# Performance work log

Hardware: AMD Instinct MI355X
Metric: run time of the kernel (lower is better)

Reference implementation:

```python
import jax, jax.numpy as jnp
import numpy as np

L = 2        # n_layers
IN = 172     # in_channels
HID = 128    # hidden_channels
NH = 4       # heads
HD = HID // NH  # per-head dim = 32
TD = 100     # time_dim
V = 400000   # global node table size
N = 150000   # sampled subgraph nodes
E = 500000   # edges per layer
B = 15000    # seed batch size


def setup_inputs() -> dict:
    key = jax.random.key(0)
    ks = jax.random.split(key, 24)
    p = lambda k, shp, s=0.05: jax.random.normal(k, shp, jnp.float32) * s
    inp = {
        "x_all": jax.random.normal(ks[0], (V, IN), jnp.float32),
        "all_node_ids": jax.random.randint(ks[1], (N,), 0, V),
        "edge_src": jax.random.randint(ks[2], (L, E), 0, N),
        "edge_dst": jax.random.randint(ks[3], (L, E), 0, N),
        "dts": jax.random.uniform(ks[4], (L, E), jnp.float32, 0.0, 1e4),
        "batch_size": B,
        # TimeEncode params
        "basis_freq": jnp.asarray(1.0 / 10 ** np.linspace(0, 9, TD), jnp.float32),
        "phase": jnp.zeros((TD,), jnp.float32),
        # input projection
        "Wp": p(ks[5], (IN, HID)), "bp": jnp.zeros((HID,), jnp.float32),
        # per-layer TransformerConv params (stacked over L)
        "Wq": p(ks[6], (L, HID, HID)), "bq": jnp.zeros((L, HID), jnp.float32),
        "Wk": p(ks[7], (L, HID, HID)), "bk": jnp.zeros((L, HID), jnp.float32),
        "Wv": p(ks[8], (L, HID, HID)), "bv": jnp.zeros((L, HID), jnp.float32),
        "We": p(ks[9], (L, TD, HID)),  # lin_edge, bias=False in PyG
        "Wskip": p(ks[10], (L, HID, HID)), "bskip": jnp.zeros((L, HID), jnp.float32),
        "bn_g": jnp.ones((L, HID), jnp.float32), "bn_b": jnp.zeros((L, HID), jnp.float32),
        # classifier head
        "W1": p(ks[11], (HID, HID)), "b1": jnp.zeros((HID,), jnp.float32),
        "g1": jnp.ones((HID,), jnp.float32), "be1": jnp.zeros((HID,), jnp.float32),
        "W2": p(ks[12], (HID, HID // 2)), "b2": jnp.zeros((HID // 2,), jnp.float32),
        "g2": jnp.ones((HID // 2,), jnp.float32), "be2": jnp.zeros((HID // 2,), jnp.float32),
        "W3": p(ks[13], (HID // 2, 1)), "b3": jnp.zeros((1,), jnp.float32),
    }
    return inp


def _bn(x, g, b):
    # BatchNorm1d, training-mode batch statistics (biased variance), eps=1e-5
    m = x.mean(0)
    v = x.var(0)
    return g * (x - m) * jax.lax.rsqrt(v + 1e-5) + b


def reference(x_all, all_node_ids, edge_src, edge_dst, dts, batch_size,
              basis_freq, phase, Wp, bp, Wq, bq, Wk, bk, Wv, bv, We,
              Wskip, bskip, bn_g, bn_b, W1, b1, g1, be1, W2, b2, g2, be2, W3, b3):
    n = all_node_ids.shape[0]
    x = x_all[all_node_ids]                      # [N, IN] gather from global table
    h = jax.nn.relu(x @ Wp + bp)                 # [N, HID]
    inv_sqrt_d = 1.0 / np.sqrt(HD)
    for i in range(L):
        src, dst, dt = edge_src[i], edge_dst[i], dts[i]
        # learnable sinusoidal time encoding of edge delta-t  [E, TD]
        te = jnp.cos(dt[:, None] * basis_freq[None, :] + phase[None, :])
        q = (h @ Wq[i] + bq[i]).reshape(n, NH, HD)
        k = (h @ Wk[i] + bk[i]).reshape(n, NH, HD)
        v = (h @ Wv[i] + bv[i]).reshape(n, NH, HD)
        e = (te @ We[i]).reshape(-1, NH, HD)     # [E, NH, HD]
        kj = k[src] + e                          # key + edge proj (PyG TransformerConv)
        vj = v[src] + e                          # value + edge proj
        alpha = jnp.einsum('ehd,ehd->eh', q[dst], kj) * inv_sqrt_d  # [E, NH]
        # scatter-softmax over edges grouped by destination node
        m = jax.ops.segment_max(alpha, dst, num_segments=n)
        a = jnp.exp(alpha - m[dst])
        s = jax.ops.segment_sum(a, dst, num_segments=n) + 1e-16
        w = a / s[dst]                           # [E, NH]
        agg = jax.ops.segment_sum(w[:, :, None] * vj, dst, num_segments=n)
        out = agg.reshape(n, HID) + h @ Wskip[i] + bskip[i]  # concat heads + root skip
        h = _bn(jax.nn.relu(out), bn_g[i], bn_b[i])          # dropout = identity (eval)
    hb = h[:batch_size]
    z = jax.nn.relu(_bn(hb @ W1 + b1, g1, be1))
    z = jax.nn.relu(_bn(z @ W2 + b2, g2, be2))
    return (z @ W3 + b3)[:, 0]                   # [batch_size]
```

## Files before the change

kernel.cpp:

```cpp
#include <hip/hip_runtime.h>
#include <hip/hip_bf16.h>
#include <math.h>

#define IN_DIM 172
#define HID 128
#define TDIM 100
#define KPAD 192

typedef __attribute__((ext_vector_type(8))) short bf16x8;
typedef __attribute__((ext_vector_type(4))) float f32x4;

static __device__ __forceinline__ ushort f2b(float x) {
  unsigned u = __float_as_uint(x);
  u += 0x7FFFu + ((u >> 16) & 1u);
  return (ushort)(u >> 16);
}
static __device__ __forceinline__ float blo(unsigned w) { return __uint_as_float(w << 16); }
static __device__ __forceinline__ float bhi(unsigned w) { return __uint_as_float(w & 0xffff0000u); }

__global__ void k_wpt(const float* __restrict__ Wp, ushort* __restrict__ wpt) {
  int i = blockIdx.x * 256 + threadIdx.x;
  if (i >= 128 * KPAD) return;
  int c = i / KPAD, k = i - c * KPAD;
  wpt[i] = (k < IN_DIM) ? f2b(Wp[k * HID + c]) : (ushort)0;
}

__global__ __launch_bounds__(256) void k_in_mfma(
    const float* __restrict__ x_all, const int* __restrict__ ids,
    const ushort* __restrict__ wpt, const float* __restrict__ bp,
    ushort* __restrict__ h, int n) {
  __shared__ __align__(16) ushort xs[64][200];
  int tid = threadIdx.x;
  long r0 = (long)blockIdx.x * 64;
  for (int i = tid; i < 64 * 28; i += 256) {
    int r = i / 28, c = IN_DIM + (i - r * 28);
    xs[r][c] = 0;
  }
  for (int i = tid; i < 64 * 43; i += 256) {
    int r = i / 43, seg = i - r * 43;
    long row = r0 + r;
    float4 v = make_float4(0.f, 0.f, 0.f, 0.f);
    if (row < n) v = *(const float4*)(x_all + (size_t)ids[row] * IN_DIM + seg * 4);
    ushort4 u;
    u.x = f2b(v.x); u.y = f2b(v.y); u.z = f2b(v.z); u.w = f2b(v.w);
    *(ushort4*)&xs[r][seg * 4] = u;
  }
  __syncthreads();
  int wv = tid >> 6, l = tid & 63;
  int arow = wv * 16 + (l & 15);
  int kb0 = (l >> 4) * 8;
  bf16x8 a[6];
  #pragma unroll
  for (int kk = 0; kk < 6; ++kk) a[kk] = *(const bf16x8*)&xs[arow][kk * 32 + kb0];
  #pragma unroll
  for (int nt = 0; nt < 8; ++nt) {
    int col = nt * 16 + (l & 15);
    const ushort* wcol = wpt + (size_t)col * KPAD + kb0;
    f32x4 acc = {0.f, 0.f, 0.f, 0.f};
    #pragma unroll
    for (int kk = 0; kk < 6; ++kk) {
      bf16x8 bfr = *(const bf16x8*)(wcol + kk * 32);
      acc = __builtin_amdgcn_mfma_f32_16x16x32_bf16(a[kk], bfr, acc, 0, 0, 0);
    }
    float bias = bp[col];
    #pragma unroll
    for (int j = 0; j < 4; ++j) {
      long row = r0 + wv * 16 + (l >> 4) * 4 + j;
      if (row < n) {
        float y = acc[j] + bias;
        h[row * HID + col] = f2b(y > 0.f ? y : 0.f);
      }
    }
  }
}

__global__ void k_wprep(const float* __restrict__ Wq, const float* __restrict__ Wk,
                        const float* __restrict__ Wv, const float* __restrict__ Ws,
                        const float* __restrict__ bq, const float* __restrict__ bk,
                        const float* __restrict__ bv, const float* __restrict__ bs,
                        ushort* __restrict__ wallT, float* __restrict__ ball) {
  int i = blockIdx.x * 256 + threadIdx.x;
  if (i >= 512 * 128) return;
  int col = i >> 7, k = i & 127;
  int m = col >> 7, c = col & 127;
  const float* W = (m == 0) ? Wq : (m == 1) ? Wk : (m == 2) ? Wv : Ws;
  wallT[i] = f2b(W[k * HID + c]);
  if (k == 0) {
    const float* bb = (m == 0) ? bq : (m == 1) ? bk : (m == 2) ? bv : bs;
    ball[col] = bb[c];
  }
}

__global__ void k_wt128(const float* __restrict__ W, ushort* __restrict__ wt) {
  int i = blockIdx.x * 256 + threadIdx.x;
  if (i >= 128 * 128) return;
  int c = i >> 7, k = i & 127;
  wt[i] = f2b(W[k * HID + c]);
}

__global__ __launch_bounds__(512) void k_qkvs(
    const ushort* __restrict__ h, const ushort* __restrict__ wallT,
    const float* __restrict__ ball,
    ushort* __restrict__ qb, ushort* __restrict__ kbuf, ushort* __restrict__ vb,
    float* __restrict__ ob, int n) {
  __shared__ __align__(16) ushort hs[128][136];
  __shared__ __align__(16) ushort ws[64][136];
  int tid = threadIdx.x;
  long r0 = (long)blockIdx.x * 128;
  bf16x8 zv = {0, 0, 0, 0, 0, 0, 0, 0};
  for (int i = tid; i < 128 * 16; i += 512) {
    int r = i >> 4, cseg = i & 15;
    long row = r0 + r;
    bf16x8 v = (row < n) ? *(const bf16x8*)&h[row * HID + cseg * 8] : zv;
    *(bf16x8*)&hs[r][cseg * 8] = v;
  }
  __syncthreads();
  int wv = tid >> 6, l = tid & 63;
  int arow = wv * 16 + (l & 15);
  int kb0 = (l >> 4) * 8;
  bf16x8 a[4];
  #pragma unroll
  for (int kk = 0; kk < 4; ++kk) a[kk] = *(const bf16x8*)&hs[arow][kk * 32 + kb0];

  for (int g = 0; g < 8; ++g) {
    __syncthreads();
    for (int i = tid; i < 64 * 16; i += 512) {
      int c = i >> 4, cseg = i & 15;
      *(bf16x8*)&ws[c][cseg * 8] =
          *(const bf16x8*)&wallT[(size_t)(g * 64 + c) * 128 + cseg * 8];
    }
    __syncthreads();
    #pragma unroll
    for (int nt = 0; nt < 4; ++nt) {
      int colc = nt * 16 + (l & 15);
      int gcol = g * 64 + colc;
      f32x4 acc = {0.f, 0.f, 0.f, 0.f};
      #pragma unroll
      for (int kk = 0; kk < 4; ++kk) {
        bf16x8 bfr = *(const bf16x8*)&ws[colc][kk * 32 + kb0];
        acc = __builtin_amdgcn_mfma_f32_16x16x32_bf16(a[kk], bfr, acc, 0, 0, 0);
      }
      float bias = ball[gcol];
      int m = gcol >> 7, c = gcol & 127;
      #pragma unroll
      for (int j = 0; j < 4; ++j) {
        long row = r0 + wv * 16 + (l >> 4) * 4 + j;
        if (row < n) {
          float y = acc[j] + bias;
          if (m == 3) ob[row * HID + c] = y;
          else {
            ushort* db = (m == 0) ? qb : (m == 1) ? kbuf : vb;
            db[row * HID + c] = f2b(y);
          }
        }
      }
    }
  }
}

__global__ __launch_bounds__(256) void k_mfma128(
    const ushort* __restrict__ X, const ushort* __restrict__ WT,
    const float* __restrict__ bias, float* __restrict__ Y, int n) {
  __shared__ __align__(16) ushort hs[64][136];
  int tid = threadIdx.x;
  long r0 = (long)blockIdx.x * 64;
  bf16x8 zv = {0, 0, 0, 0, 0, 0, 0, 0};
  for (int i = tid; i < 64 * 16; i += 256) {
    int r = i >> 4, cseg = i & 15;
    long row = r0 + r;
    bf16x8 v = (row < n) ? *(const bf16x8*)&X[row * HID + cseg * 8] : zv;
    *(bf16x8*)&hs[r][cseg * 8] = v;
  }
  __syncthreads();
  int wv = tid >> 6, l = tid & 63;
  int arow = wv * 16 + (l & 15);
  int kb0 = (l >> 4) * 8;
  bf16x8 a[4];
  #pragma unroll
  for (int kk = 0; kk < 4; ++kk) a[kk] = *(const bf16x8*)&hs[arow][kk * 32 + kb0];
  #pragma unroll
  for (int nt = 0; nt < 8; ++nt) {
    int col = nt * 16 + (l & 15);
    const ushort* wcol = WT + (size_t)col * 128 + kb0;
    f32x4 acc = {0.f, 0.f, 0.f, 0.f};
    #pragma unroll
    for (int kk = 0; kk < 4; ++kk) {
      bf16x8 bfr = *(const bf16x8*)(wcol + kk * 32);
      acc = __builtin_amdgcn_mfma_f32_16x16x32_bf16(a[kk], bfr, acc, 0, 0, 0);
    }
    float bs = bias[col];
    #pragma unroll
    for (int j = 0; j < 4; ++j) {
      long row = r0 + wv * 16 + (l >> 4) * 4 + j;
      if (row < n) Y[row * HID + col] = acc[j] + bs;
    }
  }
}

__global__ void k_hist(const int* __restrict__ dst, int* __restrict__ counts, int nE) {
  int e = blockIdx.x * 256 + threadIdx.x;
  if (e < nE) atomicAdd(&counts[dst[e]], 1);
}

__global__ void k_scan_chunk(const int* __restrict__ counts, int* __restrict__ offs,
                             int* __restrict__ chunkSums, int n) {
  __shared__ int ls[256];
  int t = threadIdx.x;
  int base = blockIdx.x * 1024 + t * 4;
  int v[4];
  #pragma unroll
  for (int j = 0; j < 4; ++j) v[j] = (base + j < n) ? counts[base + j] : 0;
  ls[t] = v[0] + v[1] + v[2] + v[3];
  __syncthreads();
  for (int off = 1; off < 256; off <<= 1) {
    int x = (t >= off) ? ls[t - off] : 0;
    __syncthreads();
    ls[t] += x;
    __syncthreads();
  }
  int run = (t == 0) ? 0 : ls[t - 1];
  if (t == 255) chunkSums[blockIdx.x] = ls[255];
  #pragma unroll
  for (int j = 0; j < 4; ++j) {
    if (base + j < n) offs[base + j] = run;
    run += v[j];
  }
}

__global__ void k_scan_tops(int* __restrict__ chunkSums, int nchunks) {
  __shared__ int ls[256];
  int t = threadIdx.x;
  ls[t] = (t < nchunks) ? chunkSums[t] : 0;
  __syncthreads();
  for (int off = 1; off < 256; off <<= 1) {
    int x = (t >= off) ? ls[t - off] : 0;
    __syncthreads();
    ls[t] += x;
    __syncthreads();
  }
  int excl = (t == 0) ? 0 : ls[t - 1];
  if (t < nchunks) chunkSums[t] = excl;
}

__global__ void k_scan_add(int* __restrict__ offs, const int* __restrict__ chunkSums,
                           int n, int nE) {
  int i = blockIdx.x * 256 + threadIdx.x;
  if (i < n) offs[i] += chunkSums[i >> 10];
  if (i == 0) offs[n] = nE;
}

__global__ void k_scatter(const int* __restrict__ src, const int* __restrict__ dst,
                          const float* __restrict__ dts, const int* __restrict__ offs,
                          int* __restrict__ cursor, int* __restrict__ src_s,
                          float* __restrict__ dts_s, int nE) {
  int e = blockIdx.x * 256 + threadIdx.x;
  if (e >= nE) return;
  int d = dst[e];
  int pos = offs[d] + atomicAdd(&cursor[d], 1);
  src_s[pos] = src[e];
  dts_s[pos] = dts[e];
}

__global__ void k_wet(const float* __restrict__ We, ushort* __restrict__ wet) {
  int i = blockIdx.x * 256 + threadIdx.x;
  if (i >= 128 * 128) return;
  int c = i >> 7, t = i & 127;
  wet[i] = (t < TDIM) ? f2b(We[t * HID + c]) : (ushort)0;
}

__global__ __launch_bounds__(256) void k_te_mfma(
    const float* __restrict__ dts, const float* __restrict__ freq,
    const float* __restrict__ phase, const ushort* __restrict__ wet,
    ushort* __restrict__ eb, int nE) {
  __shared__ __align__(16) ushort te[64][136];
  __shared__ float dt_s[64];
  __shared__ float fr_s[128], ph_s[128];
  int tid = threadIdx.x;
  if (tid < 128) {
    fr_s[tid] = (tid < TDIM) ? freq[tid] : 0.f;
    ph_s[tid] = (tid < TDIM) ? phase[tid] : 0.f;
  }
  long e0 = (long)blockIdx.x << 6;
  if (tid < 64) dt_s[tid] = (e0 + tid < nE) ? dts[e0 + tid] : 0.f;
  __syncthreads();
  for (int i = tid; i < 64 * 128; i += 256) {
    int el = i >> 7, t = i & 127;
    float val = (t < TDIM) ? __cosf(dt_s[el] * fr_s[t] + ph_s[t]) : 0.f;
    te[el][t] = f2b(val);
  }
  __syncthreads();
  int wv = tid >> 6, l = tid & 63;
  int arow = wv * 16 + (l & 15);
  int kb0 = (l >> 4) * 8;
  bf16x8 a[4];
  #pragma unroll
  for (int kk = 0; kk < 4; ++kk) a[kk] = *(const bf16x8*)&te[arow][kk * 32 + kb0];
  #pragma unroll
  for (int nt = 0; nt < 8; ++nt) {
    int col = nt * 16 + (l & 15);
    const ushort* wcol = wet + (size_t)col * 128 + kb0;
    f32x4 acc = {0.f, 0.f, 0.f, 0.f};
    #pragma unroll
    for (int kk = 0; kk < 4; ++kk) {
      bf16x8 bfr = *(const bf16x8*)(wcol + kk * 32);
      acc = __builtin_amdgcn_mfma_f32_16x16x32_bf16(a[kk], bfr, acc, 0, 0, 0);
    }
    #pragma unroll
    for (int j = 0; j < 4; ++j) {
      long row = e0 + wv * 16 + (l >> 4) * 4 + j;
      if (row < nE) eb[row * 128 + col] = f2b(acc[j]);
    }
  }
}

__global__ void k_attn(const int* __restrict__ offs, const int* __restrict__ src_s,
                       const ushort* __restrict__ eb, const ushort* __restrict__ qb,
                       const ushort* __restrict__ kb, const ushort* __restrict__ vb,
                       float* __restrict__ ob, int n) {
  int d = (blockIdx.x * 256 + threadIdx.x) >> 6;
  if (d >= n) return;
  int lane = threadIdx.x & 63;
  int half = lane >> 5;
  int cl = lane & 31;
  int c0 = cl * 4;
  int beg = offs[d], end = offs[d + 1];
  if (beg == end) return;
  uint2 qw = *(const uint2*)(qb + (size_t)d * HID + c0);
  float q0 = blo(qw.x), q1 = bhi(qw.x), q2 = blo(qw.y), q3 = bhi(qw.y);
  float m = -INFINITY, s = 0.f;
  float a0 = 0.f, a1 = 0.f, a2 = 0.f, a3 = 0.f;
  for (int base = beg; base < end; base += 2) {
    int pos = base + half;
    bool valid = pos < end;
    int pp = valid ? pos : end - 1;
    int sv = src_s[pp];
    uint2 kw = *(const uint2*)(kb + (size_t)sv * HID + c0);
    uint2 vw = *(const uint2*)(vb + (size_t)sv * HID + c0);
    uint2 ew = *(const uint2*)(eb + (size_t)pp * HID + c0);
    float e0v = blo(ew.x), e1v = bhi(ew.x), e2v = blo(ew.y), e3v = bhi(ew.y);
    float p = q0 * (blo(kw.x) + e0v) + q1 * (bhi(kw.x) + e1v) +
              q2 * (blo(kw.y) + e2v) + q3 * (bhi(kw.y) + e3v);
    p += __shfl_xor(p, 1);
    p += __shfl_xor(p, 2);
    p += __shfl_xor(p, 4);
    float aSelf = valid ? p * 0.17677669529663687f : -INFINITY;
    float aOth = __shfl_xor(aSelf, 32);
    float nm = fmaxf(m, fmaxf(aSelf, aOth));
    float sc = __expf(m - nm);
    float pe = valid ? __expf(aSelf - nm) : 0.f;
    m = nm;
    s = s * sc + pe;
    a0 = a0 * sc + pe * (blo(vw.x) + e0v);
    a1 = a1 * sc + pe * (bhi(vw.x) + e1v);
    a2 = a2 * sc + pe * (blo(vw.y) + e2v);
    a3 = a3 * sc + pe * (bhi(vw.y) + e3v);
  }
  s += __shfl_xor(s, 32);
  a0 += __shfl_xor(a0, 32);
  a1 += __shfl_xor(a1, 32);
  a2 += __shfl_xor(a2, 32);
  a3 += __shfl_xor(a3, 32);
  if (half == 0) {
    float inv = 1.f / (s + 1e-16f);
    float4* orow = (float4*)(ob + (size_t)d * HID + c0);
    float4 o = *orow;
    o.x += a0 * inv; o.y += a1 * inv; o.z += a2 * inv; o.w += a3 * inv;
    *orow = o;
  }
}

template <bool PRE_RELU>
__global__ void k_bn_reduce(const float* __restrict__ X, int n, int C, int shift,
                            float* __restrict__ sums) {
  int col = threadIdx.x & (C - 1);
  int rloc = threadIdx.x >> shift;
  int rpt = 256 >> shift;
  float s = 0.f, s2 = 0.f;
  for (long r = (long)blockIdx.x * rpt + rloc; r < n; r += (long)gridDim.x * rpt) {
    float v = X[r * C + col];
    if (PRE_RELU) v = v > 0.f ? v : 0.f;
    s += v; s2 += v * v;
  }
  __shared__ float ls[256], ls2[256];
  ls[threadIdx.x] = s; ls2[threadIdx.x] = s2;
  __syncthreads();
  if (rloc == 0) {
    for (int j = 1; j < rpt; ++j) { s += ls[j * C + col]; s2 += ls2[j * C + col]; }
    atomicAdd(&sums[col], s);
    atomicAdd(&sums[C + col], s2);
  }
}

template <bool PRE_RELU, bool POST_RELU, bool BF16OUT>
__global__ void k_bn_apply(const float* __restrict__ X, int n, int C,
                           const float* __restrict__ sums,
                           const float* __restrict__ g, const float* __restrict__ b,
                           void* __restrict__ Yv) {
  long total = (long)n * C;
  float inv_n = 1.f / (float)n;
  for (long i = (long)blockIdx.x * 256 + threadIdx.x; i < total; i += (long)gridDim.x * 256) {
    int col = (int)(i & (C - 1));
    float mean = sums[col] * inv_n;
    float var = sums[C + col] * inv_n - mean * mean;
    float v = X[i];
    if (PRE_RELU) v = v > 0.f ? v : 0.f;
    v = g[col] * (v - mean) * rsqrtf(var + 1e-5f) + b[col];
    if (POST_RELU) v = v > 0.f ? v : 0.f;
    if (BF16OUT) ((ushort*)Yv)[i] = f2b(v);
    else ((float*)Yv)[i] = v;
  }
}

__global__ __launch_bounds__(256) void k_gemm_64(
    const float* __restrict__ X, const float* __restrict__ W,
    const float* __restrict__ b, float* __restrict__ Y, int n) {
  __shared__ float xs[16][HID];
  int r0 = blockIdx.x * 16;
  for (int idx = threadIdx.x; idx < 16 * HID; idx += 256) {
    int r = idx >> 7, c = idx & 127;
    int row = r0 + r;
    xs[r][c] = (row < n) ? X[(size_t)row * HID + c] : 0.f;
  }
  __syncthreads();
  int col = threadIdx.x & 63;
  int rg = threadIdx.x >> 6;
  float acc[4] = {0.f, 0.f, 0.f, 0.f};
  #pragma unroll 4
  for (int kk = 0; kk < HID; ++kk) {
    float w = W[kk * 64 + col];
    #pragma unroll
    for (int j = 0; j < 4; ++j) acc[j] += xs[rg + 4 * j][kk] * w;
  }
  float bias = b[col];
  #pragma unroll
  for (int j = 0; j < 4; ++j) {
    int row = r0 + rg + 4 * j;
    if (row < n) Y[(size_t)row * 64 + col] = acc[j] + bias;
  }
}

__global__ __launch_bounds__(256) void k_final(
    const float* __restrict__ z2, const float* __restrict__ W3,
    const float* __restrict__ b3, float* __restrict__ out, int n) {
  int wave = threadIdx.x >> 6, lane = threadIdx.x & 63;
  int row = blockIdx.x * 4 + wave;
  if (row >= n) return;
  float pv = z2[(size_t)row * 64 + lane] * W3[lane];
  pv += __shfl_xor(pv, 1);
  pv += __shfl_xor(pv, 2);
  pv += __shfl_xor(pv, 4);
  pv += __shfl_xor(pv, 8);
  pv += __shfl_xor(pv, 16);
  pv += __shfl_xor(pv, 32);
  if (lane == 0) out[row] = pv + b3[0];
}

extern "C" void kernel_launch(void* const* d_in, const int* in_sizes, int n_in,
                              void* d_out, int out_size, void* d_ws, size_t ws_size,
                              hipStream_t stream) {
  const float* x_all = (const float*)d_in[0];
  const int* ids = (const int*)d_in[1];
  const int* esrc = (const int*)d_in[2];
  const int* edst = (const int*)d_in[3];
  const float* dts = (const float*)d_in[4];
  const float* freq = (const float*)d_in[6];
  const float* phase = (const float*)d_in[7];
  const float* Wp = (const float*)d_in[8];
  const float* bp = (const float*)d_in[9];
  const float* Wq = (const float*)d_in[10];
  const float* bq = (const float*)d_in[11];
  const float* Wk = (const float*)d_in[12];
  const float* bk = (const float*)d_in[13];
  const float* Wv = (const float*)d_in[14];
  const float* bv = (const float*)d_in[15];
  const float* We = (const float*)d_in[16];
  const float* Wskip = (const float*)d_in[17];
  const float* bskip = (const float*)d_in[18];
  const float* bn_g = (const float*)d_in[19];
  const float* bn_b = (const float*)d_in[20];
  const float* W1 = (const float*)d_in[21];
  const float* b1 = (const float*)d_in[22];
  const float* g1 = (const float*)d_in[23];
  const float* be1 = (const float*)d_in[24];
  const float* W2 = (const float*)d_in[25];
  const float* b2 = (const float*)d_in[26];
  const float* g2 = (const float*)d_in[27];
  const float* be2 = (const float*)d_in[28];
  const float* W3 = (const float*)d_in[29];
  const float* b3 = (const float*)d_in[30];

  size_t n = (size_t)in_sizes[1];
  size_t nE = (size_t)in_sizes[2] / 2;
  int B = out_size;

  char* pc = (char*)d_ws;
  auto alloc = [&](size_t bytes) { char* r = pc; pc += (bytes + 255) & ~(size_t)255; return r; };
  ushort* h    = (ushort*)alloc(n * HID * 2);
  ushort* qb   = (ushort*)alloc(n * HID * 2);
  ushort* kb   = (ushort*)alloc(n * HID * 2);
  ushort* vb   = (ushort*)alloc(n * HID * 2);
  float*  ob   = (float*)alloc(n * HID * 4);
  ushort* eb   = (ushort*)alloc(nE * HID * 2);
  int* src_s   = (int*)alloc(nE * 4);
  float* dts_s = (float*)alloc(nE * 4);
  int* counts  = (int*)alloc(n * 4);
  int* cursor  = (int*)alloc(n * 4);
  int* offs    = (int*)alloc((n + 1) * 4);
  int* chunkS  = (int*)alloc(256 * 4);
  ushort* wallT = (ushort*)alloc(512 * 128 * 2);
  float* ball  = (float*)alloc(512 * 4);
  ushort* wet  = (ushort*)alloc(128 * 128 * 2);
  ushort* w1t  = (ushort*)alloc(128 * 128 * 2);
  ushort* wpt  = (ushort*)alloc(128 * KPAD * 2);
  float* sums  = (float*)alloc(256 * 4);
  float* z1    = (float*)alloc((size_t)B * HID * 4);
  float* z2    = (float*)alloc((size_t)B * 64 * 4);

  int gn64 = (int)((n + 63) / 64);
  int gn128 = (int)((n + 127) / 128);
  int ge256 = (int)((nE + 255) / 256);
  int eblk = (int)((nE + 63) / 64);
  int nchunks = (int)((n + 1023) / 1024);

  k_wpt<<<(128 * KPAD + 255) / 256, 256, 0, stream>>>(Wp, wpt);
  k_in_mfma<<<gn64, 256, 0, stream>>>(x_all, ids, wpt, bp, h, (int)n);

  for (int i = 0; i < 2; ++i) {
    const int* src_i = esrc + i * nE;
    const int* dst_i = edst + i * nE;
    const float* dts_i = dts + i * nE;
    const float* We_i = We + (size_t)i * TDIM * HID;

    k_wprep<<<256, 256, 0, stream>>>(Wq + (size_t)i * HID * HID, Wk + (size_t)i * HID * HID,
                                     Wv + (size_t)i * HID * HID, Wskip + (size_t)i * HID * HID,
                                     bq + i * HID, bk + i * HID, bv + i * HID, bskip + i * HID,
                                     wallT, ball);
    k_qkvs<<<gn128, 512, 0, stream>>>(h, wallT, ball, qb, kb, vb, ob, (int)n);

    hipMemsetAsync(counts, 0, n * 4, stream);
    hipMemsetAsync(cursor, 0, n * 4, stream);
    k_hist<<<ge256, 256, 0, stream>>>(dst_i, counts, (int)nE);
    k_scan_chunk<<<nchunks, 256, 0, stream>>>(counts, offs, chunkS, (int)n);
    k_scan_tops<<<1, 256, 0, stream>>>(chunkS, nchunks);
    k_scan_add<<<(int)((n + 255) / 256), 256, 0, stream>>>(offs, chunkS, (int)n, (int)nE);
    k_scatter<<<ge256, 256, 0, stream>>>(src_i, dst_i, dts_i, offs, cursor, src_s, dts_s, (int)nE);

    k_wet<<<64, 256, 0, stream>>>(We_i, wet);
    k_te_mfma<<<eblk, 256, 0, stream>>>(dts_s, freq, phase, wet, eb, (int)nE);

    k_attn<<<(int)((n + 3) / 4), 256, 0, stream>>>(offs, src_s, eb, qb, kb, vb, ob, (int)n);

    hipMemsetAsync(sums, 0, 2 * HID * sizeof(float), stream);
    k_bn_reduce<true><<<512, 256, 0, stream>>>(ob, (int)n, HID, 7, sums);
    k_bn_apply<true, false, true><<<4096, 256, 0, stream>>>(ob, (int)n, HID, sums,
                                                            bn_g + i * HID, bn_b + i * HID, h);
  }

  k_wt128<<<64, 256, 0, stream>>>(W1, w1t);
  k_mfma128<<<(B + 63) / 64, 256, 0, stream>>>(h, w1t, b1, z1, B);
  hipMemsetAsync(sums, 0, 2 * HID * sizeof(float), stream);
  k_bn_reduce<false><<<512, 256, 0, stream>>>(z1, B, HID, 7, sums);
  k_bn_apply<false, true, false><<<2048, 256, 0, stream>>>(z1, B, HID, sums, g1, be1, z1);
  k_gemm_64<<<(B + 15) / 16, 256, 0, stream>>>(z1, W2, b2, z2, B);
  hipMemsetAsync(sums, 0, 2 * 64 * sizeof(float), stream);
  k_bn_reduce<false><<<512, 256, 0, stream>>>(z2, B, 64, 6, sums);
  k_bn_apply<false, true, false><<<2048, 256, 0, stream>>>(z2, B, 64, sums, g2, be2, z2);
  k_final<<<(B + 3) / 4, 256, 0, stream>>>(z2, W3, b3, (float*)d_out, B);
}
```

Before: 1.110 ms.

## Fuse BN-apply into consumers, merge weight prep, single-block scan, widen attention lanes

Folds the batch-norm apply (and its ReLU) into the next GEMM's load stage, so the separate apply passes over the node and batch activations go away. All weight transposes are merged into one prep kernel, and the memsets are merged into one. The three-kernel scan becomes a single 1024-thread block. Edge src and dt are packed into one uint2 array. Attention now handles four edges per wave with 8 channels per lane, and merges partial softmax states across lanes at the end. The cost is a serial single-block scan and extra per-block BN coefficient setup in each consumer.

New measurement: 1.599 ms. 44.1% more time.

```diff
diff --git a/kernel.cpp b/kernel.cpp
--- a/kernel.cpp
+++ b/kernel.cpp
@@ -18,11 +18,52 @@
 static __device__ __forceinline__ float blo(unsigned w) { return __uint_as_float(w << 16); }
 static __device__ __forceinline__ float bhi(unsigned w) { return __uint_as_float(w & 0xffff0000u); }
 
-__global__ void k_wpt(const float* __restrict__ Wp, ushort* __restrict__ wpt) {
+__global__ void k_prep(const float* __restrict__ Wp,
+                       const float* __restrict__ Wq, const float* __restrict__ Wk,
+                       const float* __restrict__ Wv, const float* __restrict__ Ws,
+                       const float* __restrict__ bq, const float* __restrict__ bk,
+                       const float* __restrict__ bv, const float* __restrict__ bs,
+                       const float* __restrict__ We, const float* __restrict__ W1,
+                       ushort* __restrict__ wpt,
+                       ushort* __restrict__ wallT0, ushort* __restrict__ wallT1,
+                       float* __restrict__ ball0, float* __restrict__ ball1,
+                       ushort* __restrict__ wet0, ushort* __restrict__ wet1,
+                       ushort* __restrict__ w1t) {
   int i = blockIdx.x * 256 + threadIdx.x;
-  if (i >= 128 * KPAD) return;
-  int c = i / KPAD, k = i - c * KPAD;
-  wpt[i] = (k < IN_DIM) ? f2b(Wp[k * HID + c]) : (ushort)0;
+  if (i < 128 * KPAD) {
+    int c = i / KPAD, k = i - c * KPAD;
+    wpt[i] = (k < IN_DIM) ? f2b(Wp[k * HID + c]) : (ushort)0;
+    return;
+  }
+  i -= 128 * KPAD;
+  if (i < 2 * 512 * 128) {
+    int layer = i >> 16;
+    int j = i & 65535;
+    int col = j >> 7, k = j & 127;
+    int m = col >> 7, c = col & 127;
+    const float* W = (m == 0) ? Wq : (m == 1) ? Wk : (m == 2) ? Wv : Ws;
+    W += (size_t)layer * HID * HID;
+    (layer ? wallT1 : wallT0)[j] = f2b(W[k * HID + c]);
+    if (k == 0) {
+      const float* bb = (m == 0) ? bq : (m == 1) ? bk : (m == 2) ? bv : bs;
+      (layer ? ball1 : ball0)[col] = bb[layer * HID + c];
+    }
+    return;
+  }
+  i -= 2 * 512 * 128;
+  if (i < 2 * 128 * 128) {
+    int layer = i >> 14;
+    int j = i & 16383;
+    int c = j >> 7, t = j & 127;
+    (layer ? wet1 : wet0)[j] =
+        (t < TDIM) ? f2b(We[((size_t)layer * TDIM + t) * HID + c]) : (ushort)0;
+    return;
+  }
+  i -= 2 * 128 * 128;
+  if (i < 128 * 128) {
+    int c = i >> 7, k = i & 127;
+    w1t[i] = f2b(W1[k * HID + c]);
+  }
 }
 
 __global__ __launch_bounds__(256) void k_in_mfma(
@@ -74,45 +115,55 @@
   }
 }
 
-__global__ void k_wprep(const float* __restrict__ Wq, const float* __restrict__ Wk,
-                        const float* __restrict__ Wv, const float* __restrict__ Ws,
-                        const float* __restrict__ bq, const float* __restrict__ bk,
-                        const float* __restrict__ bv, const float* __restrict__ bs,
-                        ushort* __restrict__ wallT, float* __restrict__ ball) {
-  int i = blockIdx.x * 256 + threadIdx.x;
-  if (i >= 512 * 128) return;
-  int col = i >> 7, k = i & 127;
-  int m = col >> 7, c = col & 127;
-  const float* W = (m == 0) ? Wq : (m == 1) ? Wk : (m == 2) ? Wv : Ws;
-  wallT[i] = f2b(W[k * HID + c]);
-  if (k == 0) {
-    const float* bb = (m == 0) ? bq : (m == 1) ? bk : (m == 2) ? bv : bs;
-    ball[col] = bb[c];
-  }
-}
-
-__global__ void k_wt128(const float* __restrict__ W, ushort* __restrict__ wt) {
-  int i = blockIdx.x * 256 + threadIdx.x;
-  if (i >= 128 * 128) return;
-  int c = i >> 7, k = i & 127;
-  wt[i] = f2b(W[k * HID + c]);
-}
-
+template <bool BN_IN>
 __global__ __launch_bounds__(512) void k_qkvs(
-    const ushort* __restrict__ h, const ushort* __restrict__ wallT,
-    const float* __restrict__ ball,
+    const ushort* __restrict__ hbf, const float* __restrict__ xf,
+    const float* __restrict__ sums, const float* __restrict__ bng,
+    const float* __restrict__ bnb, float inv_n,
+    const ushort* __restrict__ wallT, const float* __restrict__ ball,
     ushort* __restrict__ qb, ushort* __restrict__ kbuf, ushort* __restrict__ vb,
     float* __restrict__ ob, int n) {
   __shared__ __align__(16) ushort hs[128][136];
   __shared__ __align__(16) ushort ws[64][136];
+  __shared__ float As[128], Bs[128];
   int tid = threadIdx.x;
+  if (BN_IN) {
+    if (tid < 128) {
+      float mean = sums[tid] * inv_n;
+      float var = sums[128 + tid] * inv_n - mean * mean;
+      float A = bng[tid] * rsqrtf(var + 1e-5f);
+      As[tid] = A;
+      Bs[tid] = bnb[tid] - mean * A;
+    }
+    __syncthreads();
+  }
   long r0 = (long)blockIdx.x * 128;
-  bf16x8 zv = {0, 0, 0, 0, 0, 0, 0, 0};
   for (int i = tid; i < 128 * 16; i += 512) {
     int r = i >> 4, cseg = i & 15;
     long row = r0 + r;
-    bf16x8 v = (row < n) ? *(const bf16x8*)&h[row * HID + cseg * 8] : zv;
-    *(bf16x8*)&hs[r][cseg * 8] = v;
+    int c0 = cseg * 8;
+    if (BN_IN) {
+      ushort4 ua = {0, 0, 0, 0}, ub = {0, 0, 0, 0};
+      if (row < n) {
+        const float* xr = xf + row * HID + c0;
+        float4 xa = *(const float4*)xr;
+        float4 xb = *(const float4*)(xr + 4);
+        ua.x = f2b(As[c0 + 0] * fmaxf(xa.x, 0.f) + Bs[c0 + 0]);
+        ua.y = f2b(As[c0 + 1] * fmaxf(xa.y, 0.f) + Bs[c0 + 1]);
+        ua.z = f2b(As[c0 + 2] * fmaxf(xa.z, 0.f) + Bs[c0 + 2]);
+        ua.w = f2b(As[c0 + 3] * fmaxf(xa.w, 0.f) + Bs[c0 + 3]);
+        ub.x = f2b(As[c0 + 4] * fmaxf(xb.x, 0.f) + Bs[c0 + 4]);
+        ub.y = f2b(As[c0 + 5] * fmaxf(xb.y, 0.f) + Bs[c0 + 5]);
+        ub.z = f2b(As[c0 + 6] * fmaxf(xb.z, 0.f) + Bs[c0 + 6]);
+        ub.w = f2b(As[c0 + 7] * fmaxf(xb.w, 0.f) + Bs[c0 + 7]);
+      }
+      *(ushort4*)&hs[r][c0] = ua;
+      *(ushort4*)&hs[r][c0 + 4] = ub;
+    } else {
+      bf16x8 zv = {0, 0, 0, 0, 0, 0, 0, 0};
+      bf16x8 v = (row < n) ? *(const bf16x8*)&hbf[row * HID + c0] : zv;
+      *(bf16x8*)&hs[r][c0] = v;
+    }
   }
   __syncthreads();
   int wv = tid >> 6, l = tid & 63;
@@ -158,18 +209,43 @@
   }
 }
 
-__global__ __launch_bounds__(256) void k_mfma128(
-    const ushort* __restrict__ X, const ushort* __restrict__ WT,
-    const float* __restrict__ bias, float* __restrict__ Y, int n) {
+__global__ __launch_bounds__(256) void k_mfma128_bn(
+    const float* __restrict__ xf, const float* __restrict__ sums,
+    const float* __restrict__ bng, const float* __restrict__ bnb, float inv_n,
+    const ushort* __restrict__ WT, const float* __restrict__ bias,
+    float* __restrict__ Y, int n) {
   __shared__ __align__(16) ushort hs[64][136];
+  __shared__ float As[128], Bs[128];
   int tid = threadIdx.x;
+  if (tid < 128) {
+    float mean = sums[tid] * inv_n;
+    float var = sums[128 + tid] * inv_n - mean * mean;
+    float A = bng[tid] * rsqrtf(var + 1e-5f);
+    As[tid] = A;
+    Bs[tid] = bnb[tid] - mean * A;
+  }
+  __syncthreads();
   long r0 = (long)blockIdx.x * 64;
-  bf16x8 zv = {0, 0, 0, 0, 0, 0, 0, 0};
   for (int i = tid; i < 64 * 16; i += 256) {
     int r = i >> 4, cseg = i & 15;
     long row = r0 + r;
-    bf16x8 v = (row < n) ? *(const bf16x8*)&X[row * HID + cseg * 8] : zv;
-    *(bf16x8*)&hs[r][cseg * 8] = v;
+    int c0 = cseg * 8;
+    ushort4 ua = {0, 0, 0, 0}, ub = {0, 0, 0, 0};
+    if (row < n) {
+      const float* xr = xf + row * HID + c0;
+      float4 xa = *(const float4*)xr;
+      float4 xb = *(const float4*)(xr + 4);
+      ua.x = f2b(As[c0 + 0] * fmaxf(xa.x, 0.f) + Bs[c0 + 0]);
+      ua.y = f2b(As[c0 + 1] * fmaxf(xa.y, 0.f) + Bs[c0 + 1]);
+      ua.z = f2b(As[c0 + 2] * fmaxf(xa.z, 0.f) + Bs[c0 + 2]);
+      ua.w = f2b(As[c0 + 3] * fmaxf(xa.w, 0.f) + Bs[c0 + 3]);
+      ub.x = f2b(As[c0 + 4] * fmaxf(xb.x, 0.f) + Bs[c0 + 4]);
+      ub.y = f2b(As[c0 + 5] * fmaxf(xb.y, 0.f) + Bs[c0 + 5]);
+      ub.z = f2b(As[c0 + 6] * fmaxf(xb.z, 0.f) + Bs[c0 + 6]);
+      ub.w = f2b(As[c0 + 7] * fmaxf(xb.w, 0.f) + Bs[c0 + 7]);
+    }
+    *(ushort4*)&hs[r][c0] = ua;
+    *(ushort4*)&hs[r][c0 + 4] = ub;
   }
   __syncthreads();
   int wv = tid >> 6, l = tid & 63;
@@ -202,74 +278,48 @@
   if (e < nE) atomicAdd(&counts[dst[e]], 1);
 }
 
-__global__ void k_scan_chunk(const int* __restrict__ counts, int* __restrict__ offs,
-                             int* __restrict__ chunkSums, int n) {
-  __shared__ int ls[256];
+__global__ __launch_bounds__(1024) void k_scan(const int* __restrict__ counts,
+                                               int* __restrict__ offs, int n, int nE) {
+  __shared__ int ls[1024];
   int t = threadIdx.x;
-  int base = blockIdx.x * 1024 + t * 4;
-  int v[4];
-  #pragma unroll
-  for (int j = 0; j < 4; ++j) v[j] = (base + j < n) ? counts[base + j] : 0;
-  ls[t] = v[0] + v[1] + v[2] + v[3];
-  __syncthreads();
-  for (int off = 1; off < 256; off <<= 1) {
+  int chunk = (n + 1023) >> 10;
+  int b0 = t * chunk;
+  int sum = 0;
+  for (int j = 0; j < chunk; ++j) {
+    int idx = b0 + j;
+    if (idx < n) sum += counts[idx];
+  }
+  ls[t] = sum;
+  __syncthreads();
+  for (int off = 1; off < 1024; off <<= 1) {
     int x = (t >= off) ? ls[t - off] : 0;
     __syncthreads();
     ls[t] += x;
     __syncthreads();
   }
   int run = (t == 0) ? 0 : ls[t - 1];
-  if (t == 255) chunkSums[blockIdx.x] = ls[255];
-  #pragma unroll
-  for (int j = 0; j < 4; ++j) {
-    if (base + j < n) offs[base + j] = run;
-    run += v[j];
-  }
-}
-
-__global__ void k_scan_tops(int* __restrict__ chunkSums, int nchunks) {
-  __shared__ int ls[256];
-  int t = threadIdx.x;
-  ls[t] = (t < nchunks) ? chunkSums[t] : 0;
-  __syncthreads();
-  for (int off = 1; off < 256; off <<= 1) {
-    int x = (t >= off) ? ls[t - off] : 0;
-    __syncthreads();
-    ls[t] += x;
-    __syncthreads();
-  }
-  int excl = (t == 0) ? 0 : ls[t - 1];
-  if (t < nchunks) chunkSums[t] = excl;
-}
-
-__global__ void k_scan_add(int* __restrict__ offs, const int* __restrict__ chunkSums,
-                           int n, int nE) {
-  int i = blockIdx.x * 256 + threadIdx.x;
-  if (i < n) offs[i] += chunkSums[i >> 10];
-  if (i == 0) offs[n] = nE;
+  for (int j = 0; j < chunk; ++j) {
+    int idx = b0 + j;
+    if (idx < n) {
+      offs[idx] = run;
+      run += counts[idx];
+    }
+  }
+  if (t == 0) offs[n] = nE;
 }
 
 __global__ void k_scatter(const int* __restrict__ src, const int* __restrict__ dst,
                           const float* __restrict__ dts, const int* __restrict__ offs,
-                          int* __restrict__ cursor, int* __restrict__ src_s,
-                          float* __restrict__ dts_s, int nE) {
+                          int* __restrict__ cursor, uint2* __restrict__ edata, int nE) {
   int e = blockIdx.x * 256 + threadIdx.x;
   if (e >= nE) return;
   int d = dst[e];
   int pos = offs[d] + atomicAdd(&cursor[d], 1);
-  src_s[pos] = src[e];
-  dts_s[pos] = dts[e];
-}
-
-__global__ void k_wet(const float* __restrict__ We, ushort* __restrict__ wet) {
-  int i = blockIdx.x * 256 + threadIdx.x;
-  if (i >= 128 * 128) return;
-  int c = i >> 7, t = i & 127;
-  wet[i] = (t < TDIM) ? f2b(We[t * HID + c]) : (ushort)0;
+  edata[pos] = make_uint2((unsigned)src[e], __float_as_uint(dts[e]));
 }
 
 __global__ __launch_bounds__(256) void k_te_mfma(
-    const float* __restrict__ dts, const float* __restrict__ freq,
+    const uint2* __restrict__ edata, const float* __restrict__ freq,
     const float* __restrict__ phase, const ushort* __restrict__ wet,
     ushort* __restrict__ eb, int nE) {
   __shared__ __align__(16) ushort te[64][136];
@@ -281,7 +331,7 @@
     ph_s[tid] = (tid < TDIM) ? phase[tid] : 0.f;
   }
   long e0 = (long)blockIdx.x << 6;
-  if (tid < 64) dt_s[tid] = (e0 + tid < nE) ? dts[e0 + tid] : 0.f;
+  if (tid < 64) dt_s[tid] = (e0 + tid < nE) ? __uint_as_float(edata[e0 + tid].y) : 0.f;
   __syncthreads();
   for (int i = tid; i < 64 * 128; i += 256) {
     int el = i >> 7, t = i & 127;
@@ -313,59 +363,79 @@
   }
 }
 
-__global__ void k_attn(const int* __restrict__ offs, const int* __restrict__ src_s,
+__global__ void k_attn(const int* __restrict__ offs, const uint2* __restrict__ edata,
                        const ushort* __restrict__ eb, const ushort* __restrict__ qb,
                        const ushort* __restrict__ kb, const ushort* __restrict__ vb,
                        float* __restrict__ ob, int n) {
   int d = (blockIdx.x * 256 + threadIdx.x) >> 6;
   if (d >= n) return;
   int lane = threadIdx.x & 63;
-  int half = lane >> 5;
-  int cl = lane & 31;
-  int c0 = cl * 4;
+  int sub = lane >> 4;
+  int cl = lane & 15;
+  int c0 = cl * 8;
   int beg = offs[d], end = offs[d + 1];
   if (beg == end) return;
-  uint2 qw = *(const uint2*)(qb + (size_t)d * HID + c0);
+  uint4 qw = *(const uint4*)(qb + (size_t)d * HID + c0);
   float q0 = blo(qw.x), q1 = bhi(qw.x), q2 = blo(qw.y), q3 = bhi(qw.y);
+  float q4 = blo(qw.z), q5 = bhi(qw.z), q6 = blo(qw.w), q7 = bhi(qw.w);
   float m = -INFINITY, s = 0.f;
-  float a0 = 0.f, a1 = 0.f, a2 = 0.f, a3 = 0.f;
-  for (int base = beg; base < end; base += 2) {
-    int pos = base + half;
+  float a0 = 0.f, a1 = 0.f, a2 = 0.f, a3 = 0.f, a4 = 0.f, a5 = 0.f, a6 = 0.f, a7 = 0.f;
+  for (int base = beg; base < end; base += 4) {
+    int pos = base + sub;
     bool valid = pos < end;
-    int pp = valid ? pos : end - 1;
-    int sv = src_s[pp];
-    uint2 kw = *(const uint2*)(kb + (size_t)sv * HID + c0);
-    uint2 vw = *(const uint2*)(vb + (size_t)sv * HID + c0);
-    uint2 ew = *(const uint2*)(eb + (size_t)pp * HID + c0);
-    float e0v = blo(ew.x), e1v = bhi(ew.x), e2v = blo(ew.y), e3v = bhi(ew.y);
-    float p = q0 * (blo(kw.x) + e0v) + q1 * (bhi(kw.x) + e1v) +
-              q2 * (blo(kw.y) + e2v) + q3 * (bhi(kw.y) + e3v);
+    int pp = valid ? pos : beg;
+    int sv = (int)edata[pp].x;
+    uint4 kw = *(const uint4*)(kb + (size_t)sv * HID + c0);
+    uint4 vw = *(const uint4*)(vb + (size_t)sv * HID + c0);
+    uint4 ew = *(const uint4*)(eb + (size_t)pp * HID + c0);
+    float e0 = blo(ew.x), e1 = bhi(ew.x), e2 = blo(ew.y), e3 = bhi(ew.y);
+    float e4 = blo(ew.z), e5 = bhi(ew.z), e6 = blo(ew.w), e7 = bhi(ew.w);
+    float p = q0 * (blo(kw.x) + e0) + q1 * (bhi(kw.x) + e1) +
+              q2 * (blo(kw.y) + e2) + q3 * (bhi(kw.y) + e3) +
+              q4 * (blo(kw.z) + e4) + q5 * (bhi(kw.z) + e5) +
+              q6 * (blo(kw.w) + e6) + q7 * (bhi(kw.w) + e7);
     p += __shfl_xor(p, 1);
     p += __shfl_xor(p, 2);
-    p += __shfl_xor(p, 4);
-    float aSelf = valid ? p * 0.17677669529663687f : -INFINITY;
-    float aOth = __shfl_xor(aSelf, 32);
-    float nm = fmaxf(m, fmaxf(aSelf, aOth));
-    float sc = __expf(m - nm);
-    float pe = valid ? __expf(aSelf - nm) : 0.f;
+    float av = valid ? p * 0.17677669529663687f : -INFINITY;
+    float nm = fmaxf(m, av);
+    float sc = (m > -INFINITY) ? __expf(m - nm) : 0.f;
+    float pe = valid ? __expf(av - nm) : 0.f;
     m = nm;
     s = s * sc + pe;
-    a0 = a0 * sc + pe * (blo(vw.x) + e0v);
-    a1 = a1 * sc + pe * (bhi(vw.x) + e1v);
-    a2 = a2 * sc + pe * (blo(vw.y) + e2v);
-    a3 = a3 * sc + pe * (bhi(vw.y) + e3v);
-  }
-  s += __shfl_xor(s, 32);
-  a0 += __shfl_xor(a0, 32);
-  a1 += __shfl_xor(a1, 32);
-  a2 += __shfl_xor(a2, 32);
-  a3 += __shfl_xor(a3, 32);
-  if (half == 0) {
+    a0 = a0 * sc + pe * (blo(vw.x) + e0);
+    a1 = a1 * sc + pe * (bhi(vw.x) + e1);
+    a2 = a2 * sc + pe * (blo(vw.y) + e2);
+    a3 = a3 * sc + pe * (bhi(vw.y) + e3);
+    a4 = a4 * sc + pe * (blo(vw.z) + e4);
+    a5 = a5 * sc + pe * (bhi(vw.z) + e5);
+    a6 = a6 * sc + pe * (blo(vw.w) + e6);
+    a7 = a7 * sc + pe * (bhi(vw.w) + e7);
+  }
+  #pragma unroll
+  for (int off = 16; off <= 32; off <<= 1) {
+    float mo = __shfl_xor(m, off);
+    float so = __shfl_xor(s, off);
+    float t0 = __shfl_xor(a0, off), t1 = __shfl_xor(a1, off);
+    float t2 = __shfl_xor(a2, off), t3 = __shfl_xor(a3, off);
+    float t4 = __shfl_xor(a4, off), t5 = __shfl_xor(a5, off);
+    float t6 = __shfl_xor(a6, off), t7 = __shfl_xor(a7, off);
+    float nm = fmaxf(m, mo);
+    float s1 = (m > -INFINITY) ? __expf(m - nm) : 0.f;
+    float s2 = (mo > -INFINITY) ? __expf(mo - nm) : 0.f;
+    s = s * s1 + so * s2;
+    a0 = a0 * s1 + t0 * s2; a1 = a1 * s1 + t1 * s2;
+    a2 = a2 * s1 + t2 * s2; a3 = a3 * s1 + t3 * s2;
+    a4 = a4 * s1 + t4 * s2; a5 = a5 * s1 + t5 * s2;
+    a6 = a6 * s1 + t6 * s2; a7 = a7 * s1 + t7 * s2;
+    m = nm;
+  }
+  if (sub == 0) {
     float inv = 1.f / (s + 1e-16f);
-    float4* orow = (float4*)(ob + (size_t)d * HID + c0);
-    float4 o = *orow;
-    o.x += a0 * inv; o.y += a1 * inv; o.z += a2 * inv; o.w += a3 * inv;
-    *orow = o;
+    float4* o = (float4*)(ob + (size_t)d * HID + c0);
+    float4 x0 = o[0], x1 = o[1];
+    x0.x += a0 * inv; x0.y += a1 * inv; x0.z += a2 * inv; x0.w += a3 * inv;
+    x1.x += a4 * inv; x1.y += a5 * inv; x1.z += a6 * inv; x1.w += a7 * inv;
+    o[0] = x0; o[1] = x1;
   }
 }
 
@@ -391,35 +461,29 @@
   }
 }
 
-template <bool PRE_RELU, bool POST_RELU, bool BF16OUT>
-__global__ void k_bn_apply(const float* __restrict__ X, int n, int C,
-                           const float* __restrict__ sums,
-                           const float* __restrict__ g, const float* __restrict__ b,
-                           void* __restrict__ Yv) {
-  long total = (long)n * C;
-  float inv_n = 1.f / (float)n;
-  for (long i = (long)blockIdx.x * 256 + threadIdx.x; i < total; i += (long)gridDim.x * 256) {
-    int col = (int)(i & (C - 1));
-    float mean = sums[col] * inv_n;
-    float var = sums[C + col] * inv_n - mean * mean;
-    float v = X[i];
-    if (PRE_RELU) v = v > 0.f ? v : 0.f;
-    v = g[col] * (v - mean) * rsqrtf(var + 1e-5f) + b[col];
-    if (POST_RELU) v = v > 0.f ? v : 0.f;
-    if (BF16OUT) ((ushort*)Yv)[i] = f2b(v);
-    else ((float*)Yv)[i] = v;
-  }
-}
-
 __global__ __launch_bounds__(256) void k_gemm_64(
-    const float* __restrict__ X, const float* __restrict__ W,
-    const float* __restrict__ b, float* __restrict__ Y, int n) {
+    const float* __restrict__ X, const float* __restrict__ sums,
+    const float* __restrict__ g, const float* __restrict__ be, float inv_n,
+    const float* __restrict__ W, const float* __restrict__ b,
+    float* __restrict__ Y, int n) {
   __shared__ float xs[16][HID];
+  __shared__ float As[128], Bs[128];
+  if (threadIdx.x < 128) {
+    int c = threadIdx.x;
+    float mean = sums[c] * inv_n;
+    float var = sums[128 + c] * inv_n - mean * mean;
+    float A = g[c] * rsqrtf(var + 1e-5f);
+    As[c] = A;
+    Bs[c] = be[c] - mean * A;
+  }
+  __syncthreads();
   int r0 = blockIdx.x * 16;
   for (int idx = threadIdx.x; idx < 16 * HID; idx += 256) {
     int r = idx >> 7, c = idx & 127;
     int row = r0 + r;
-    xs[r][c] = (row < n) ? X[(size_t)row * HID + c] : 0.f;
+    float v = (row < n) ? X[(size_t)row * HID + c] : 0.f;
+    v = As[c] * v + Bs[c];
+    xs[r][c] = v > 0.f ? v : 0.f;
   }
   __syncthreads();
   int col = threadIdx.x & 63;
@@ -440,12 +504,19 @@
 }
 
 __global__ __launch_bounds__(256) void k_final(
-    const float* __restrict__ z2, const float* __restrict__ W3,
-    const float* __restrict__ b3, float* __restrict__ out, int n) {
+    const float* __restrict__ z2, const float* __restrict__ sums,
+    const float* __restrict__ g2, const float* __restrict__ be2, float inv_n,
+    const float* __restrict__ W3, const float* __restrict__ b3,
+    float* __restrict__ out, int n) {
   int wave = threadIdx.x >> 6, lane = threadIdx.x & 63;
   int row = blockIdx.x * 4 + wave;
   if (row >= n) return;
-  float pv = z2[(size_t)row * 64 + lane] * W3[lane];
+  float z = z2[(size_t)row * 64 + lane];
+  float mean = sums[lane] * inv_n;
+  float var = sums[64 + lane] * inv_n - mean * mean;
+  float v = g2[lane] * (z - mean) * rsqrtf(var + 1e-5f) + be2[lane];
+  v = v > 0.f ? v : 0.f;
+  float pv = v * W3[lane];
   pv += __shfl_xor(pv, 1);
   pv += __shfl_xor(pv, 2);
   pv += __shfl_xor(pv, 4);
@@ -499,71 +570,76 @@
   ushort* qb   = (ushort*)alloc(n * HID * 2);
   ushort* kb   = (ushort*)alloc(n * HID * 2);
   ushort* vb   = (ushort*)alloc(n * HID * 2);
-  float*  ob   = (float*)alloc(n * HID * 4);
+  float*  ob0  = (float*)alloc(n * HID * 4);
+  float*  ob1  = (float*)alloc(n * HID * 4);
   ushort* eb   = (ushort*)alloc(nE * HID * 2);
-  int* src_s   = (int*)alloc(nE * 4);
-  float* dts_s = (float*)alloc(nE * 4);
-  int* counts  = (int*)alloc(n * 4);
-  int* cursor  = (int*)alloc(n * 4);
+  uint2* edata = (uint2*)alloc(nE * 8);
   int* offs    = (int*)alloc((n + 1) * 4);
-  int* chunkS  = (int*)alloc(256 * 4);
-  ushort* wallT = (ushort*)alloc(512 * 128 * 2);
-  float* ball  = (float*)alloc(512 * 4);
-  ushort* wet  = (ushort*)alloc(128 * 128 * 2);
-  ushort* w1t  = (ushort*)alloc(128 * 128 * 2);
-  ushort* wpt  = (ushort*)alloc(128 * KPAD * 2);
-  float* sums  = (float*)alloc(256 * 4);
-  float* z1    = (float*)alloc((size_t)B * HID * 4);
-  float* z2    = (float*)alloc((size_t)B * 64 * 4);
+  size_t zbytes = 4 * n * 4 + 4 * 256 * 4;
+  char* zb = alloc(zbytes);
+  int* counts0 = (int*)zb;
+  int* cursor0 = counts0 + n;
+  int* counts1 = cursor0 + n;
+  int* cursor1 = counts1 + n;
+  float* sumsL0 = (float*)(cursor1 + n);
+  float* sumsL1 = sumsL0 + 256;
+  float* sumsZ1 = sumsL1 + 256;
+  float* sumsZ2 = sumsZ1 + 256;
+  ushort* wpt    = (ushort*)alloc(128 * KPAD * 2);
+  ushort* wallT0 = (ushort*)alloc(512 * 128 * 2);
+  ushort* wallT1 = (ushort*)alloc(512 * 128 * 2);
+  float* ball0   = (float*)alloc(512 * 4);
+  float* ball1   = (float*)alloc(512 * 4);
+  ushort* wet0   = (ushort*)alloc(128 * 128 * 2);
+  ushort* wet1   = (ushort*)alloc(128 * 128 * 2);
+  ushort* w1t    = (ushort*)alloc(128 * 128 * 2);
+  float* z1      = (float*)alloc((size_t)B * HID * 4);
+  float* z2      = (float*)alloc((size_t)B * 64 * 4);
 
   int gn64 = (int)((n + 63) / 64);
   int gn128 = (int)((n + 127) / 128);
   int ge256 = (int)((nE + 255) / 256);
   int eblk = (int)((nE + 63) / 64);
-  int nchunks = (int)((n + 1023) / 1024);
-
-  k_wpt<<<(128 * KPAD + 255) / 256, 256, 0, stream>>>(Wp, wpt);
+  float inv_nf = 1.f / (float)n;
+  float inv_bf = 1.f / (float)B;
+
+  hipMemsetAsync(zb, 0, zbytes, stream);
+  k_prep<<<(128 * KPAD + 2 * 512 * 128 + 2 * 128 * 128 + 128 * 128 + 255) / 256, 256, 0, stream>>>(
+      Wp, Wq, Wk, Wv, Wskip, bq, bk, bv, bskip, We, W1,
+      wpt, wallT0, wallT1, ball0, ball1, wet0, wet1, w1t);
   k_in_mfma<<<gn64, 256, 0, stream>>>(x_all, ids, wpt, bp, h, (int)n);
 
   for (int i = 0; i < 2; ++i) {
     const int* src_i = esrc + i * nE;
     const int* dst_i = edst + i * nE;
     const float* dts_i = dts + i * nE;
-    const float* We_i = We + (size_t)i * TDIM * HID;
-
-    k_wprep<<<256, 256, 0, stream>>>(Wq + (size_t)i * HID * HID, Wk + (size_t)i * HID * HID,
-                                     Wv + (size_t)i * HID * HID, Wskip + (size_t)i * HID * HID,
-                                     bq + i * HID, bk + i * HID, bv + i * HID, bskip + i * HID,
-                                     wallT, ball);
-    k_qkvs<<<gn128, 512, 0, stream>>>(h, wallT, ball, qb, kb, vb, ob, (int)n);
-
-    hipMemsetAsync(counts, 0, n * 4, stream);
-    hipMemsetAsync(cursor, 0, n * 4, stream);
+    int* counts = i ? counts1 : counts0;
+    int* cursor = i ? cursor1 : cursor0;
+    const ushort* wallT = i ? wallT1 : wallT0;
+    const float* ball = i ? ball1 : ball0;
+    const ushort* wet = i ? wet1 : wet0;
+    float* ob = i ? ob1 : ob0;
+
+    if (i == 0)
+      k_qkvs<false><<<gn128, 512, 0, stream>>>(h, nullptr, nullptr, nullptr, nullptr, 0.f,
+                                               wallT, ball, qb, kb, vb, ob, (int)n);
+    else
+      k_qkvs<true><<<gn128, 512, 0, stream>>>(nullptr, ob0, sumsL0, bn_g, bn_b, inv_nf,
+                                              wallT, ball, qb, kb, vb, ob, (int)n);
+
     k_hist<<<ge256, 256, 0, stream>>>(dst_i, counts, (int)nE);
-    k_scan_chunk<<<nchunks, 256, 0, stream>>>(counts, offs, chunkS, (int)n);
-    k_scan_tops<<<1, 256, 0, stream>>>(chunkS, nchunks);
-    k_scan_add<<<(int)((n + 255) / 256), 256, 0, stream>>>(offs, chunkS, (int)n, (int)nE);
-    k_scatter<<<ge256, 256, 0, stream>>>(src_i, dst_i, dts_i, offs, cursor, src_s, dts_s, (int)nE);
-
-    k_wet<<<64, 256, 0, stream>>>(We_i, wet);
-    k_te_mfma<<<eblk, 256, 0, stream>>>(dts_s, freq, phase, wet, eb, (int)nE);
-
-    k_attn<<<(int)((n + 3) / 4), 256, 0, stream>>>(offs, src_s, eb, qb, kb, vb, ob, (int)n);
-
-    hipMemsetAsync(sums, 0, 2 * HID * sizeof(float), stream);
-    k_bn_reduce<true><<<512, 256, 0, stream>>>(ob, (int)n, HID, 7, sums);
-    k_bn_apply<true, false, true><<<4096, 256, 0, stream>>>(ob, (int)n, HID, sums,
-                                                            bn_g + i * HID, bn_b + i * HID, h);
-  }
-
-  k_wt128<<<64, 256, 0, stream>>>(W1, w1t);
-  k_mfma128<<<(B + 63) / 64, 256, 0, stream>>>(h, w1t, b1, z1, B);
-  hipMemsetAsync(sums, 0, 2 * HID * sizeof(float), stream);
-  k_bn_reduce<false><<<512, 256, 0, stream>>>(z1, B, HID, 7, sums);
-  k_bn_apply<false, true, false><<<2048, 256, 0, stream>>>(z1, B, HID, sums, g1, be1, z1);
-  k_gemm_64<<<(B + 15) / 16, 256, 0, stream>>>(z1, W2, b2, z2, B);
-  hipMemsetAsync(sums, 0, 2 * 64 * sizeof(float), stream);
-  k_bn_reduce<false><<<512, 256, 0, stream>>>(z2, B, 64, 6, sums);
-  k_bn_apply<false, true, false><<<2048, 256, 0, stream>>>(z2, B, 64, sums, g2, be2, z2);
-  k_final<<<(B + 3) / 4, 256, 0, stream>>>(z2, W3, b3, (float*)d_out, B);
-}
+    k_scan<<<1, 1024, 0, stream>>>(counts, offs, (int)n, (int)nE);
+    k_scatter<<<ge256, 256, 0, stream>>>(src_i, dst_i, dts_i, offs, cursor, edata, (int)nE);
+    k_te_mfma<<<eblk, 256, 0, stream>>>(edata, freq, phase, wet, eb, (int)nE);
+    k_attn<<<(int)((n + 3) / 4), 256, 0, stream>>>(offs, edata, eb, qb, kb, vb, ob, (int)n);
+    k_bn_reduce<true><<<512, 256, 0, stream>>>(ob, (int)n, HID, 7, i ? sumsL1 : sumsL0);
+  }
+
+  k_mfma128_bn<<<(B + 63) / 64, 256, 0, stream>>>(ob1, sumsL1, bn_g + HID, bn_b + HID,
+                                                  inv_nf, w1t, b1, z1, B);
+  k_bn_reduce<false><<<512, 256, 0, stream>>>(z1, B, HID, 7, sumsZ1);
+  k_gemm_64<<<(B + 15) / 16, 256, 0, stream>>>(z1, sumsZ1, g1, be1, inv_bf, W2, b2, z2, B);
+  k_bn_reduce<false><<<512, 256, 0, stream>>>(z2, B, 64, 6, sumsZ2);
+  k_final<<<(B + 3) / 4, 256, 0, stream>>>(z2, sumsZ2, g2, be2, inv_bf, W3, b3,
+                                           (float*)d_out, B);
+}
```
